# Kernel optimization log

Measured on AMD Instinct MI355X. Metric: run time of the kernel, lower is better.

Reference implementation:

```python
import jax, jax.numpy as jnp
import numpy as np

B, T, DIM, H, HD, K = 4, 2048, 1024, 16, 64, 4
QK = H * HD          # 1024
VD = 2 * H * HD      # 2048
EPS = 1e-5


def zrms(x, g):
    # zero-centered RMS norm with learned scale
    x = x - jnp.mean(x, axis=-1, keepdims=True)
    return x * jax.lax.rsqrt(jnp.mean(x * x, axis=-1, keepdims=True) + EPS) * g


def causal_dwconv(x, w):
    # x: [B,T,C], w: [K,1,C] (keras depthwise Conv1D kernel, groups=C)
    k = w.shape[0]
    return jax.lax.conv_general_dilated(
        x, w, window_strides=(1,), padding=[(k - 1, 0)],
        dimension_numbers=('NWC', 'WIO', 'NWC'),
        feature_group_count=x.shape[-1])


def setup_inputs() -> dict:
    key = jax.random.key(0)
    ks = jax.random.split(key, 12)
    s = lambda *sh: 1.0 / np.sqrt(sh[0])
    return {
        'x':  jax.random.normal(ks[0], (B, T, DIM), jnp.float32),
        'Wq': jax.random.normal(ks[1], (DIM, QK), jnp.float32) * s(DIM),
        'Wk': jax.random.normal(ks[2], (DIM, QK), jnp.float32) * s(DIM),
        'Wv': jax.random.normal(ks[3], (DIM, VD), jnp.float32) * s(DIM),
        'gq': jnp.ones((QK,), jnp.float32),
        'gk': jnp.ones((QK,), jnp.float32),
        'gv': jnp.ones((VD,), jnp.float32),
        'cq': jax.random.normal(ks[4], (K, 1, QK), jnp.float32) * 0.5,
        'ck': jax.random.normal(ks[5], (K, 1, QK), jnp.float32) * 0.5,
        'cv': jax.random.normal(ks[6], (K, 1, VD), jnp.float32) * 0.5,
        'Wa': jax.random.normal(ks[7], (DIM, H), jnp.float32) * s(DIM),
        'Wb': jax.random.normal(ks[8], (DIM, H), jnp.float32) * s(DIM),
        'Wo': jax.random.normal(ks[9], (VD, DIM), jnp.float32) * s(VD),
        'Wg': jax.random.normal(ks[10], (DIM, DIM), jnp.float32) * s(DIM),
    }


def reference(x, Wq, Wk, Wv, gq, gk, gv, cq, ck, cv, Wa, Wb, Wo, Wg):
    # 1) projections  2) zero-centered RMSNorm  3) causal depthwise conv (+silu)
    q = jax.nn.silu(causal_dwconv(zrms(x @ Wq, gq), cq))   # [B,T,QK]
    k = jax.nn.silu(causal_dwconv(zrms(x @ Wk, gk), ck))   # [B,T,QK]
    v = jax.nn.silu(causal_dwconv(zrms(x @ Wv, gv), cv))   # [B,T,VD]

    q = q.reshape(B, T, H, HD)
    k = k.reshape(B, T, H, HD)
    v = v.reshape(B, T, H, 2 * HD)

    # 4) per-head gating params
    alpha = jax.nn.sigmoid(x @ Wa)  # [B,T,H]
    beta = jax.nn.sigmoid(x @ Wb)   # [B,T,H]

    # 5) gated delta-rule recurrence over time (state S: [B,H,2*HD,HD])
    def step(S, inp):
        qt, kt, vt, at, bt = inp  # [B,H,HD],[B,H,HD],[B,H,2HD],[B,H],[B,H]
        a = at[..., None, None]
        upd = S + bt[..., None, None] * jnp.einsum('bhv,bhk->bhvk', vt, kt)
        S = a * upd + (1.0 - a) * S
        o = jnp.einsum('bhvk,bhk->bhv', S, qt)  # Q_t readout
        return S, o

    S0 = jnp.zeros((B, H, 2 * HD, HD), x.dtype)
    xs = (q.transpose(1, 0, 2, 3), k.transpose(1, 0, 2, 3),
          v.transpose(1, 0, 2, 3), alpha.transpose(1, 0, 2),
          beta.transpose(1, 0, 2))
    _, o = jax.lax.scan(step, S0, xs)          # o: [T,B,H,2HD]
    o = o.transpose(1, 0, 2, 3).reshape(B, T, VD)

    # 6) output projection + sigmoid output gate
    proj = o @ Wo                              # [B,T,DIM]
    return jax.nn.sigmoid(proj @ Wg) * proj
```

## Files before the change

### kernel.cpp

```cpp
#include <hip/hip_runtime.h>
#include <hip/hip_bf16.h>
#include <math.h>

#define RTOT 8192
#define TSEQ 2048

typedef __attribute__((ext_vector_type(8))) short short8;
typedef __attribute__((ext_vector_type(4))) float f32x4;
typedef unsigned short u16;
typedef unsigned int u32;

union U16x8 { uint4 v; u16 s[8]; };

__device__ __forceinline__ float sigmoidf_(float x) { return 1.f / (1.f + expf(-x)); }
__device__ __forceinline__ float bf2f(u16 v) { u32 u = ((u32)v) << 16; float f; __builtin_memcpy(&f, &u, 4); return f; }
__device__ __forceinline__ u16 f2bf(float f) {
  u32 u; __builtin_memcpy(&u, &f, 4);
  u32 r = (u + 0x7FFFu + ((u >> 16) & 1u)) >> 16;
  return (u16)r;
}
__device__ __forceinline__ void split2(float x, u16& h, u16& l) {
  u16 hh = f2bf(x);
  float hf = bf2f(hh);
  h = hh; l = f2bf(x - hf);
}

typedef const void __attribute__((address_space(1))) gvoid_t;
typedef void __attribute__((address_space(3))) lvoid_t;
__device__ __forceinline__ void gload_lds16(const void* g, void* l) {
  __builtin_amdgcn_global_load_lds((gvoid_t*)g, (lvoid_t*)l, 16, 0, 0);
}

__device__ __forceinline__ void xcd_remap(int& bx, int& by) {
  int gx = gridDim.x, nwg = gx * gridDim.y;
  int bid = blockIdx.y * gx + blockIdx.x;
  int cpx = nwg >> 3;
  int swz = (bid & 7) * cpx + (bid >> 3);
  bx = swz % gx; by = swz / gx;
}

template<int EPI>
__global__ __launch_bounds__(256) void gemm_sp(const u16* __restrict__ Ah, const u16* __restrict__ Al,
                                               const u16* __restrict__ Bh, const u16* __restrict__ Bl,
                                               float* __restrict__ Cf, u16* __restrict__ Ph,
                                               u16* __restrict__ Pl, const float* __restrict__ Pin,
                                               int M, int N, int K) {
  __shared__ u16 Ash[128 * 32], Asl[128 * 32];
  __shared__ u16 Bsh[128 * 32], Bsl[128 * 32];
  int bx, by; xcd_remap(bx, by);
  const int tid = threadIdx.x;
  const int l = tid & 63, w = tid >> 6;
  const int m0 = by * 128, n0 = bx * 128;
  const int wr = w >> 1, wc = w & 1;
  f32x4 acc[4][4] = {};
  const int srow = (w << 5) + (l >> 2);
  const int scol = (l & 3) << 3;
  const size_t gA = (size_t)(m0 + srow) * K + scol;
  const size_t gB = (size_t)(n0 + srow) * K + scol;
  const int lo0 = (w * 2 + 0) * 512, lo1 = (w * 2 + 1) * 512;
  const int arow = wr * 64 + (l & 15), brow = wc * 64 + (l & 15);
  const int koff = 8 * (l >> 4);
  for (int k0 = 0; k0 < K; k0 += 32) {
    gload_lds16(Ah + gA + k0, &Ash[lo0]);
    gload_lds16(Ah + gA + 16 * K + k0, &Ash[lo1]);
    gload_lds16(Al + gA + k0, &Asl[lo0]);
    gload_lds16(Al + gA + 16 * K + k0, &Asl[lo1]);
    gload_lds16(Bh + gB + k0, &Bsh[lo0]);
    gload_lds16(Bh + gB + 16 * K + k0, &Bsh[lo1]);
    gload_lds16(Bl + gB + k0, &Bsl[lo0]);
    gload_lds16(Bl + gB + 16 * K + k0, &Bsl[lo1]);
    __syncthreads();
    short8 afh[4], afl[4], bfh[4], bfl[4];
#pragma unroll
    for (int m = 0; m < 4; ++m) {
      afh[m] = *(const short8*)&Ash[(arow + m * 16) * 32 + koff];
      afl[m] = *(const short8*)&Asl[(arow + m * 16) * 32 + koff];
    }
#pragma unroll
    for (int n = 0; n < 4; ++n) {
      bfh[n] = *(const short8*)&Bsh[(brow + n * 16) * 32 + koff];
      bfl[n] = *(const short8*)&Bsl[(brow + n * 16) * 32 + koff];
    }
#pragma unroll
    for (int m = 0; m < 4; ++m)
#pragma unroll
      for (int n = 0; n < 4; ++n) {
        acc[m][n] = __builtin_amdgcn_mfma_f32_16x16x32_bf16(afh[m], bfh[n], acc[m][n], 0, 0, 0);
        acc[m][n] = __builtin_amdgcn_mfma_f32_16x16x32_bf16(afh[m], bfl[n], acc[m][n], 0, 0, 0);
        acc[m][n] = __builtin_amdgcn_mfma_f32_16x16x32_bf16(afl[m], bfh[n], acc[m][n], 0, 0, 0);
      }
    __syncthreads();
  }
  const int rbase = m0 + wr * 64 + 4 * (l >> 4);
  const int cbase = n0 + wc * 64 + (l & 15);
#pragma unroll
  for (int m = 0; m < 4; ++m)
#pragma unroll
    for (int n = 0; n < 4; ++n)
#pragma unroll
      for (int r = 0; r < 4; ++r) {
        size_t idx = (size_t)(rbase + m * 16 + r) * N + (cbase + n * 16);
        float v = acc[m][n][r];
        if (EPI == 0) {
          Cf[idx] = v;
        } else if (EPI == 1) {
          Cf[idx] = v;
          u16 h, lo; split2(v, h, lo);
          Ph[idx] = h; Pl[idx] = lo;
        } else {
          Cf[idx] = Pin[idx] * sigmoidf_(v);
        }
      }
}

__global__ __launch_bounds__(256) void transcast_sp(const float* __restrict__ W,
                                                    u16* __restrict__ Wth, u16* __restrict__ Wtl,
                                                    int K, int N) {
  __shared__ float t[32][33];
  const int n0 = blockIdx.x * 32, k0 = blockIdx.y * 32;
  const int c = threadIdx.x & 31, rq = threadIdx.x >> 5;
#pragma unroll
  for (int i = 0; i < 4; ++i) t[rq * 4 + i][c] = W[(size_t)(k0 + rq * 4 + i) * N + n0 + c];
  __syncthreads();
#pragma unroll
  for (int i = 0; i < 4; ++i) {
    float v = t[c][rq * 4 + i];
    u16 h, lo; split2(v, h, lo);
    size_t idx = (size_t)(n0 + rq * 4 + i) * K + k0 + c;
    Wth[idx] = h; Wtl[idx] = lo;
  }
}

__global__ __launch_bounds__(256) void castx_sp(const float* __restrict__ x,
                                                u16* __restrict__ xh, u16* __restrict__ xl) {
  size_t i = (size_t)blockIdx.x * 256 + threadIdx.x;
  float4 v = ((const float4*)x)[i];
  ushort4 hh, ll;
  split2(v.x, hh.x, ll.x); split2(v.y, hh.y, ll.y);
  split2(v.z, hh.z, ll.z); split2(v.w, hh.w, ll.w);
  ((ushort4*)xh)[i] = hh; ((ushort4*)xl)[i] = ll;
}

template<int C, int GSCALE>
__global__ __launch_bounds__(C / 4) void conv_fs(const float* __restrict__ zn,
                                                 const float* __restrict__ w,
                                                 const float* __restrict__ g,
                                                 const float* __restrict__ gab,
                                                 u16* __restrict__ oh,
                                                 u16* __restrict__ ol) {
  constexpr int NW = C / 256;
  __shared__ float redA[NW * 4];
  __shared__ float redB[NW * 4];
  const int tid = threadIdx.x;
  const int row = blockIdx.x;
  const int t = row & (TSEQ - 1);
  const int c = tid * 4;
  const int lane = tid & 63, wid = tid >> 6;
  float4 xv[4];
  float psum[4];
#pragma unroll
  for (int d = 0; d < 4; ++d) {
    if (t - d >= 0) xv[d] = *(const float4*)(zn + (size_t)(row - d) * 4096 + c);
    else { xv[d].x = 0.f; xv[d].y = 0.f; xv[d].z = 0.f; xv[d].w = 0.f; }
    psum[d] = xv[d].x + xv[d].y + xv[d].z + xv[d].w;
  }
#pragma unroll
  for (int d = 0; d < 4; ++d)
#pragma unroll
    for (int o = 32; o > 0; o >>= 1) psum[d] += __shfl_xor(psum[d], o, 64);
  if (lane == 0) {
    redA[wid * 4 + 0] = psum[0]; redA[wid * 4 + 1] = psum[1];
    redA[wid * 4 + 2] = psum[2]; redA[wid * 4 + 3] = psum[3];
  }
  __syncthreads();
  float mean[4];
#pragma unroll
  for (int d = 0; d < 4; ++d) {
    float s = 0.f;
#pragma unroll
    for (int j = 0; j < NW; ++j) s += redA[j * 4 + d];
    mean[d] = s * (1.f / C);
  }
  float psq[4];
#pragma unroll
  for (int d = 0; d < 4; ++d) {
    float a = xv[d].x - mean[d], b = xv[d].y - mean[d];
    float e = xv[d].z - mean[d], f = xv[d].w - mean[d];
    psq[d] = a * a + b * b + e * e + f * f;
  }
#pragma unroll
  for (int d = 0; d < 4; ++d)
#pragma unroll
    for (int o = 32; o > 0; o >>= 1) psq[d] += __shfl_xor(psq[d], o, 64);
  if (lane == 0) {
    redB[wid * 4 + 0] = psq[0]; redB[wid * 4 + 1] = psq[1];
    redB[wid * 4 + 2] = psq[2]; redB[wid * 4 + 3] = psq[3];
  }
  __syncthreads();
  float rstd[4];
#pragma unroll
  for (int d = 0; d < 4; ++d) {
    float s = 0.f;
#pragma unroll
    for (int j = 0; j < NW; ++j) s += redB[j * 4 + d];
    rstd[d] = rsqrtf(s * (1.f / C) + 1e-5f);
  }
  float4 g4 = *(const float4*)(g + c);
  float4 acc; acc.x = 0.f; acc.y = 0.f; acc.z = 0.f; acc.w = 0.f;
#pragma unroll
  for (int d = 0; d < 4; ++d) {
    if (t - d >= 0) {
      float4 wv = *(const float4*)(w + (size_t)(3 - d) * C + c);
      acc.x = fmaf((xv[d].x - mean[d]) * rstd[d] * g4.x, wv.x, acc.x);
      acc.y = fmaf((xv[d].y - mean[d]) * rstd[d] * g4.y, wv.y, acc.y);
      acc.z = fmaf((xv[d].z - mean[d]) * rstd[d] * g4.z, wv.z, acc.z);
      acc.w = fmaf((xv[d].w - mean[d]) * rstd[d] * g4.w, wv.w, acc.w);
    }
  }
  float a0 = acc.x * sigmoidf_(acc.x);
  float a1 = acc.y * sigmoidf_(acc.y);
  float a2 = acc.z * sigmoidf_(acc.z);
  float a3 = acc.w * sigmoidf_(acc.w);
  if (GSCALE) {
    float gv = gab[(size_t)row * 16 + (c >> 7)];
    a0 *= gv; a1 *= gv; a2 *= gv; a3 *= gv;
  }
  ushort4 hh, ll;
  split2(a0, hh.x, ll.x); split2(a1, hh.y, ll.y);
  split2(a2, hh.z, ll.z); split2(a3, hh.w, ll.w);
  *(ushort4*)(oh + (size_t)row * C + c) = hh;
  *(ushort4*)(ol + (size_t)row * C + c) = ll;
}

__global__ __launch_bounds__(256) void gab_kernel(const float* __restrict__ x,
                                                  const float* __restrict__ Wa,
                                                  const float* __restrict__ Wb,
                                                  float* __restrict__ gout) {
  __shared__ float xs[1024];
  __shared__ float partial[256];
  const int tid = threadIdx.x;
  const size_t row = blockIdx.x;
  *(float4*)(&xs[tid*4]) = *(const float4*)(x + row*1024 + tid*4);
  __syncthreads();
  const int h = tid & 31;
  const int seg = tid >> 5;
  const float* W = (h < 16) ? Wa : Wb;
  const int col = h & 15;
  float s = 0.f;
  const int k0 = seg * 128;
  for (int k = 0; k < 128; ++k) s = fmaf(xs[k0 + k], W[(size_t)(k0 + k) * 16 + col], s);
  partial[tid] = s;
  __syncthreads();
  if (tid < 32) {
    float t2 = 0.f;
#pragma unroll
    for (int j = 0; j < 8; ++j) t2 += partial[j*32 + tid];
    partial[tid] = t2;
  }
  __syncthreads();
  if (tid < 16)
    gout[row*16 + tid] = sigmoidf_(partial[tid]) * sigmoidf_(partial[tid + 16]);
}

__global__ __launch_bounds__(256) void scan_kernel(const u16* __restrict__ kh,
                                                   const u16* __restrict__ kl,
                                                   const u16* __restrict__ vgh,
                                                   const u16* __restrict__ vgl,
                                                   u16* __restrict__ Sph,
                                                   u16* __restrict__ Spl) {
  __shared__ float Ks[64][36];
  __shared__ float Vs[64][36];
  const int tid = threadIdx.x;
  const int bid = blockIdx.x;
  const int kq = bid & 1, vq = (bid >> 1) & 3, h = (bid >> 3) & 15, b = bid >> 7;
  const size_t rb = (size_t)b * TSEQ;
  const int vd_t = tid >> 3, kd0 = (tid & 7) * 4;
  float S[4] = {};
  const int sr = tid >> 2;
  const int cc0 = (tid & 3) * 8;
  for (int c = 0; c < 32; ++c) {
    {
      size_t koffg = (rb + (size_t)c * 64 + sr) * 1024 + h * 64 + kq * 32 + cc0;
      U16x8 a0, b0;
      a0.v = *(const uint4*)(kh + koffg);
      b0.v = *(const uint4*)(kl + koffg);
#pragma unroll
      for (int j = 0; j < 8; ++j) Ks[sr][cc0 + j] = bf2f(a0.s[j]) + bf2f(b0.s[j]);
      size_t voffg = (rb + (size_t)c * 64 + sr) * 2048 + h * 128 + vq * 32 + cc0;
      U16x8 va, vb;
      va.v = *(const uint4*)(vgh + voffg);
      vb.v = *(const uint4*)(vgl + voffg);
#pragma unroll
      for (int j = 0; j < 8; ++j) Vs[sr][cc0 + j] = bf2f(va.s[j]) + bf2f(vb.s[j]);
    }
    {
      size_t spc = (((size_t)(b * 16 + h) * 32) + c) * 8192
                 + (size_t)(vq * 32 + vd_t) * 64 + kq * 32 + kd0;
      ushort4 h0, l0;
      split2(S[0], h0.x, l0.x); split2(S[1], h0.y, l0.y);
      split2(S[2], h0.z, l0.z); split2(S[3], h0.w, l0.w);
      *(ushort4*)(Sph + spc) = h0;
      *(ushort4*)(Spl + spc) = l0;
    }
    __syncthreads();
    for (int s = 0; s < 64; ++s) {
      float vv = Vs[s][vd_t];
      float kv[4];
      *(float4*)kv = *(const float4*)&Ks[s][kd0];
#pragma unroll
      for (int j = 0; j < 4; ++j) S[j] = fmaf(vv, kv[j], S[j]);
    }
    __syncthreads();
  }
}

__global__ __launch_bounds__(256) void pass2_sp(const u16* __restrict__ qh,
                                                const u16* __restrict__ ql,
                                                const u16* __restrict__ kh,
                                                const u16* __restrict__ vgh,
                                                const u16* __restrict__ Sph,
                                                const u16* __restrict__ Spl,
                                                u16* __restrict__ oh,
                                                u16* __restrict__ ol) {
  __shared__ u16 Qsh[64 * 72];
  __shared__ u16 Qsl[64 * 72];
  __shared__ u16 Ksm[64 * 72];
  __shared__ u16 Am[64 * 72];
  __shared__ u16 Vth[128 * 72];
  const int tid = threadIdx.x;
  const int l = tid & 63, w = tid >> 6;
  const int bid = blockIdx.x;
  const int c = bid & 31, h = (bid >> 5) & 15, b = bid >> 9;
  const size_t rb = (size_t)b * TSEQ + c * 64;
  const int fr = l & 15, fq = l >> 4;
  {
    int r = tid >> 2, c0 = (tid & 3) * 16;
    size_t off = (rb + r) * 1024 + h * 64 + c0;
    *(uint4*)&Qsh[r * 72 + c0]     = *(const uint4*)(qh + off);
    *(uint4*)&Qsh[r * 72 + c0 + 8] = *(const uint4*)(qh + off + 8);
    *(uint4*)&Qsl[r * 72 + c0]     = *(const uint4*)(ql + off);
    *(uint4*)&Qsl[r * 72 + c0 + 8] = *(const uint4*)(ql + off + 8);
    *(uint4*)&Ksm[r * 72 + c0]     = *(const uint4*)(kh + off);
    *(uint4*)&Ksm[r * 72 + c0 + 8] = *(const uint4*)(kh + off + 8);
  }
  {
    int s = tid >> 2, vd0 = (tid & 3) * 32;
    size_t off = (rb + s) * 2048 + h * 128 + vd0;
#pragma unroll
    for (int m4 = 0; m4 < 4; ++m4) {
      U16x8 r_; r_.v = *(const uint4*)(vgh + off + m4 * 8);
#pragma unroll
      for (int j = 0; j < 8; ++j) Vth[(vd0 + m4 * 8 + j) * 72 + s] = r_.s[j];
    }
  }
  __syncthreads();
  short8 aqh[2], aql[2];
#pragma unroll
  for (int kk = 0; kk < 2; ++kk) {
    aqh[kk] = *(const short8*)&Qsh[(w * 16 + fr) * 72 + kk * 32 + 8 * fq];
    aql[kk] = *(const short8*)&Qsl[(w * 16 + fr) * 72 + kk * 32 + 8 * fq];
  }
  f32x4 accA[4] = {};
#pragma unroll
  for (int n = 0; n < 4; ++n)
#pragma unroll
    for (int kk = 0; kk < 2; ++kk) {
      short8 bk = *(const short8*)&Ksm[(n * 16 + fr) * 72 + kk * 32 + 8 * fq];
      accA[n] = __builtin_amdgcn_mfma_f32_16x16x32_bf16(aqh[kk], bk, accA[n], 0, 0, 0);
    }
#pragma unroll
  for (int n = 0; n < 4; ++n)
#pragma unroll
    for (int rr = 0; rr < 4; ++rr) {
      int tt = w * 16 + 4 * fq + rr;
      int s = n * 16 + fr;
      Am[tt * 72 + s] = f2bf((s <= tt) ? accA[n][rr] : 0.f);
    }
  __syncthreads();
  f32x4 acc[8] = {};
#pragma unroll
  for (int kk = 0; kk < 2; ++kk) {
    short8 aa = *(const short8*)&Am[(w * 16 + fr) * 72 + kk * 32 + 8 * fq];
#pragma unroll
    for (int n = 0; n < 8; ++n) {
      short8 bv = *(const short8*)&Vth[(n * 16 + fr) * 72 + kk * 32 + 8 * fq];
      acc[n] = __builtin_amdgcn_mfma_f32_16x16x32_bf16(aa, bv, acc[n], 0, 0, 0);
    }
  }
  const size_t spb = (((size_t)(b * 16 + h) * 32) + c) * 8192;
#pragma unroll
  for (int n = 0; n < 8; ++n)
#pragma unroll
    for (int kk = 0; kk < 2; ++kk) {
      size_t soff = spb + (size_t)(n * 16 + fr) * 64 + kk * 32 + 8 * fq;
      short8 bh_ = *(const short8*)(Sph + soff);
      short8 bl_ = *(const short8*)(Spl + soff);
      acc[n] = __builtin_amdgcn_mfma_f32_16x16x32_bf16(aqh[kk], bh_, acc[n], 0, 0, 0);
      acc[n] = __builtin_amdgcn_mfma_f32_16x16x32_bf16(aqh[kk], bl_, acc[n], 0, 0, 0);
      acc[n] = __builtin_amdgcn_mfma_f32_16x16x32_bf16(aql[kk], bh_, acc[n], 0, 0, 0);
    }
#pragma unroll
  for (int n = 0; n < 8; ++n)
#pragma unroll
    for (int rr = 0; rr < 4; ++rr) {
      int tt = w * 16 + 4 * fq + rr;
      int vd = n * 16 + fr;
      u16 hh, ll;
      split2(acc[n][rr], hh, ll);
      size_t off = (rb + tt) * 2048 + h * 128 + vd;
      oh[off] = hh; ol[off] = ll;
    }
}

extern "C" void kernel_launch(void* const* d_in, const int* in_sizes, int n_in,
                              void* d_out, int out_size, void* d_ws, size_t ws_size,
                              hipStream_t stream) {
  (void)in_sizes; (void)n_in; (void)out_size; (void)ws_size;
  const float* x  = (const float*)d_in[0];
  const float* Wq = (const float*)d_in[1];
  const float* Wk = (const float*)d_in[2];
  const float* Wv = (const float*)d_in[3];
  const float* gq = (const float*)d_in[4];
  const float* gk = (const float*)d_in[5];
  const float* gv = (const float*)d_in[6];
  const float* cq = (const float*)d_in[7];
  const float* ck = (const float*)d_in[8];
  const float* cv = (const float*)d_in[9];
  const float* Wa = (const float*)d_in[10];
  const float* Wb = (const float*)d_in[11];
  const float* Wo = (const float*)d_in[12];
  const float* Wg = (const float*)d_in[13];
  float* out = (float*)d_out;
  char* ws = (char*)d_ws;

  const size_t MiB = 1024 * 1024;
  u16* Wqkv_h = (u16*)(ws + 0 * MiB);
  u16* Wqkv_l = (u16*)(ws + 8 * MiB);
  u16* Wo_h   = (u16*)(ws + 16 * MiB);
  u16* Wo_l   = (u16*)(ws + 20 * MiB);
  u16* Wg_h   = (u16*)(ws + 24 * MiB);
  u16* Wg_l   = (u16*)(ws + 26 * MiB);
  float* gbuf = (float*)(ws + 28 * MiB);
  u16* x_h    = (u16*)(ws + 32 * MiB);
  u16* x_l    = (u16*)(ws + 48 * MiB);
  float* qkv  = (float*)(ws + 64 * MiB);
  u16* q_h = (u16*)(ws + 192 * MiB);
  u16* q_l = (u16*)(ws + 208 * MiB);
  u16* k_h = (u16*)(ws + 224 * MiB);
  u16* k_l = (u16*)(ws + 240 * MiB);
  u16* vg_h = (u16*)(ws + 32 * MiB);
  u16* vg_l = (u16*)d_out;
  u16* Sp_h = (u16*)(ws + 96 * MiB);
  u16* Sp_l = (u16*)(ws + 128 * MiB);
  u16* o_h  = (u16*)(ws + 64 * MiB);
  u16* o_l  = (u16*)d_out;
  float* proj = (float*)(ws + 96 * MiB);
  u16* p_h  = (u16*)(ws + 128 * MiB);
  u16* p_l  = (u16*)(ws + 144 * MiB);

  dim3 blk(256);
  castx_sp<<<dim3(8192), blk, 0, stream>>>(x, x_h, x_l);
  transcast_sp<<<dim3(32, 32), blk, 0, stream>>>(Wq, Wqkv_h, Wqkv_l, 1024, 1024);
  transcast_sp<<<dim3(32, 32), blk, 0, stream>>>(Wk, Wqkv_h + 1024 * 1024, Wqkv_l + 1024 * 1024, 1024, 1024);
  transcast_sp<<<dim3(64, 32), blk, 0, stream>>>(Wv, Wqkv_h + 2048 * 1024, Wqkv_l + 2048 * 1024, 1024, 2048);
  transcast_sp<<<dim3(32, 64), blk, 0, stream>>>(Wo, Wo_h, Wo_l, 2048, 1024);
  transcast_sp<<<dim3(32, 32), blk, 0, stream>>>(Wg, Wg_h, Wg_l, 1024, 1024);
  gab_kernel<<<dim3(8192), blk, 0, stream>>>(x, Wa, Wb, gbuf);
  gemm_sp<0><<<dim3(32, 64), blk, 0, stream>>>(x_h, x_l, Wqkv_h, Wqkv_l, qkv, nullptr, nullptr, nullptr, 8192, 4096, 1024);
  conv_fs<1024, 0><<<dim3(8192), dim3(256), 0, stream>>>(qkv, cq, gq, nullptr, q_h, q_l);
  conv_fs<1024, 0><<<dim3(8192), dim3(256), 0, stream>>>(qkv + 1024, ck, gk, nullptr, k_h, k_l);
  conv_fs<2048, 1><<<dim3(8192), dim3(512), 0, stream>>>(qkv + 2048, cv, gv, gbuf, vg_h, vg_l);
  scan_kernel<<<dim3(512), blk, 0, stream>>>(k_h, k_l, vg_h, vg_l, Sp_h, Sp_l);
  pass2_sp<<<dim3(2048), blk, 0, stream>>>(q_h, q_l, k_h, vg_h, Sp_h, Sp_l, o_h, o_l);
  gemm_sp<1><<<dim3(8, 64), blk, 0, stream>>>(o_h, o_l, Wo_h, Wo_l, proj, p_h, p_l, nullptr, 8192, 1024, 2048);
  gemm_sp<2><<<dim3(8, 64), blk, 0, stream>>>(p_h, p_l, Wg_h, Wg_l, out, nullptr, nullptr, proj, 8192, 1024, 1024);
}
```

Baseline: 718.0 us.

## Use 256x256 double-buffered split-bf16 GEMM kernel for QKV projection

Adds a dedicated 512-thread GEMM for the QKV projection that uses 256x256 output tiles, with each wave computing 128x64. It double-buffers the hi/lo A and B tiles in LDS using async global-to-LDS loads, and raises wave priority around the MFMA block. The larger tile gives more arithmetic per byte loaded and overlaps the loads for the next tile with compute. The costs are 128KB of LDS per block, which leaves one block per CU, and heavy register use from 32 accumulators.

```diff
diff --git a/kernel.cpp b/kernel.cpp
--- a/kernel.cpp
+++ b/kernel.cpp
@@ -37,6 +37,89 @@
   int cpx = nwg >> 3;
   int swz = (bid & 7) * cpx + (bid >> 3);
   bx = swz % gx; by = swz / gx;
+}
+
+__global__ __launch_bounds__(512) void gemm_sp_big(const u16* __restrict__ Ah, const u16* __restrict__ Al,
+                                                   const u16* __restrict__ Bh, const u16* __restrict__ Bl,
+                                                   float* __restrict__ Cf,
+                                                   int M, int N, int K) {
+  __shared__ u16 lds[2][4][256 * 32];
+  int bx, by; xcd_remap(bx, by);
+  const int tid = threadIdx.x;
+  const int l = tid & 63, w = tid >> 6;
+  const int wr = w >> 2, wc = w & 3;
+  const int m0 = by * 256, n0 = bx * 256;
+  const int fr = l & 15, fq = l >> 4;
+  const int koff = 8 * fq;
+  const int srow = tid >> 2, scol = (tid & 3) * 8;
+  const u16* gA_h = Ah + (size_t)(m0 + srow) * K + scol;
+  const u16* gA_l = Al + (size_t)(m0 + srow) * K + scol;
+  const u16* gB_h = Bh + (size_t)(n0 + srow) * K + scol;
+  const u16* gB_l = Bl + (size_t)(n0 + srow) * K + scol;
+  const int lo = srow * 32 + scol;
+  const int NT = K >> 5;
+
+#define STAGE_QKV(buf, t)                                            \
+  do {                                                               \
+    const int k0_ = (t) << 5;                                        \
+    gload_lds16(gA_h + k0_, &lds[buf][0][lo]);                       \
+    gload_lds16(gA_h + 128 * K + k0_, &lds[buf][0][lo + 4096]);      \
+    gload_lds16(gA_l + k0_, &lds[buf][1][lo]);                       \
+    gload_lds16(gA_l + 128 * K + k0_, &lds[buf][1][lo + 4096]);      \
+    gload_lds16(gB_h + k0_, &lds[buf][2][lo]);                       \
+    gload_lds16(gB_h + 128 * K + k0_, &lds[buf][2][lo + 4096]);      \
+    gload_lds16(gB_l + k0_, &lds[buf][3][lo]);                       \
+    gload_lds16(gB_l + 128 * K + k0_, &lds[buf][3][lo + 4096]);      \
+  } while (0)
+
+  f32x4 acc[8][4] = {};
+  STAGE_QKV(0, 0);
+  STAGE_QKV(1, 1);
+  asm volatile("s_waitcnt vmcnt(8)" ::: "memory");
+  __builtin_amdgcn_s_barrier();
+
+  for (int t = 0; t < NT; ++t) {
+    const int cur = t & 1;
+    short8 bh8[4], bl8[4];
+#pragma unroll
+    for (int n = 0; n < 4; ++n) {
+      bh8[n] = *(const short8*)&lds[cur][2][(wc * 64 + n * 16 + fr) * 32 + koff];
+      bl8[n] = *(const short8*)&lds[cur][3][(wc * 64 + n * 16 + fr) * 32 + koff];
+    }
+    short8 ah8[8], al8[8];
+#pragma unroll
+    for (int m = 0; m < 8; ++m) {
+      ah8[m] = *(const short8*)&lds[cur][0][(wr * 128 + m * 16 + fr) * 32 + koff];
+      al8[m] = *(const short8*)&lds[cur][1][(wr * 128 + m * 16 + fr) * 32 + koff];
+    }
+    asm volatile("s_waitcnt lgkmcnt(0)" ::: "memory");
+    __builtin_amdgcn_s_barrier();
+    if (t + 2 < NT) STAGE_QKV(cur, t + 2);
+    __builtin_amdgcn_s_setprio(1);
+#pragma unroll
+    for (int m = 0; m < 8; ++m)
+#pragma unroll
+      for (int n = 0; n < 4; ++n) {
+        acc[m][n] = __builtin_amdgcn_mfma_f32_16x16x32_bf16(ah8[m], bh8[n], acc[m][n], 0, 0, 0);
+        acc[m][n] = __builtin_amdgcn_mfma_f32_16x16x32_bf16(ah8[m], bl8[n], acc[m][n], 0, 0, 0);
+        acc[m][n] = __builtin_amdgcn_mfma_f32_16x16x32_bf16(al8[m], bh8[n], acc[m][n], 0, 0, 0);
+      }
+    __builtin_amdgcn_s_setprio(0);
+    if (t + 2 < NT) {
+      asm volatile("s_waitcnt vmcnt(8)" ::: "memory");
+    } else if (t + 1 < NT) {
+      asm volatile("s_waitcnt vmcnt(0)" ::: "memory");
+    }
+    __builtin_amdgcn_s_barrier();
+  }
+#undef STAGE_QKV
+#pragma unroll
+  for (int m = 0; m < 8; ++m)
+#pragma unroll
+    for (int n = 0; n < 4; ++n)
+#pragma unroll
+      for (int r = 0; r < 4; ++r)
+        Cf[(size_t)(m0 + wr * 128 + m * 16 + 4 * fq + r) * N + (n0 + wc * 64 + n * 16 + fr)] = acc[m][n][r];
 }
 
 template<int EPI>
@@ -466,7 +549,7 @@
   transcast_sp<<<dim3(32, 64), blk, 0, stream>>>(Wo, Wo_h, Wo_l, 2048, 1024);
   transcast_sp<<<dim3(32, 32), blk, 0, stream>>>(Wg, Wg_h, Wg_l, 1024, 1024);
   gab_kernel<<<dim3(8192), blk, 0, stream>>>(x, Wa, Wb, gbuf);
-  gemm_sp<0><<<dim3(32, 64), blk, 0, stream>>>(x_h, x_l, Wqkv_h, Wqkv_l, qkv, nullptr, nullptr, nullptr, 8192, 4096, 1024);
+  gemm_sp_big<<<dim3(16, 32), dim3(512), 0, stream>>>(x_h, x_l, Wqkv_h, Wqkv_l, qkv, 8192, 4096, 1024);
   conv_fs<1024, 0><<<dim3(8192), dim3(256), 0, stream>>>(qkv, cq, gq, nullptr, q_h, q_l);
   conv_fs<1024, 0><<<dim3(8192), dim3(256), 0, stream>>>(qkv + 1024, ck, gk, nullptr, k_h, k_l);
   conv_fs<2048, 1><<<dim3(8192), dim3(512), 0, stream>>>(qkv + 2048, cv, gv, gbuf, vg_h, vg_l);
```

Measured after the change: 692.2 us. -3.6%, faster.
